# Performance work log

Measured on AMD Instinct MI355X. Metric: run time of the kernel, lower is better.

The kernel has to match this reference:

```python
import jax, jax.numpy as jnp
import numpy as np

N_NODES = 50000
N_EDGES = 800000
IN_C, HID_C, OUT_C = 256, 256, 128


def gcn_conv(x, W, b, row, col, n_nodes):
    """PyG GCNConv: linear transform, symmetric-normalized aggregation, bias.
    row/col already include self-loops. Messages flow row -> col."""
    h = x @ W  # [N, out]
    deg = jax.ops.segment_sum(jnp.ones_like(col, dtype=h.dtype), col, num_segments=n_nodes)
    d_inv_sqrt = jnp.where(deg > 0, jax.lax.rsqrt(jnp.maximum(deg, 1e-12)), 0.0)
    norm = d_inv_sqrt[row] * d_inv_sqrt[col]  # [E]
    msg = h[row] * norm[:, None]              # gather + scale, [E, out]
    out = jax.ops.segment_sum(msg, col, num_segments=n_nodes)  # scatter-add
    return out + b


def setup_inputs() -> dict:
    key = jax.random.key(0)
    k_x, k_e, k_w1, k_w2 = jax.random.split(key, 4)
    x = jax.random.normal(k_x, (N_NODES, IN_C), dtype=jnp.float32)
    edge_index = jax.random.randint(k_e, (2, N_EDGES), 0, N_NODES, dtype=jnp.int64)
    # Glorot-style init for GCN weights, zeros bias (PyG default)
    s1 = float(np.sqrt(6.0 / (IN_C + HID_C)))
    s2 = float(np.sqrt(6.0 / (HID_C + OUT_C)))
    W1 = jax.random.uniform(k_w1, (IN_C, HID_C), dtype=jnp.float32, minval=-s1, maxval=s1)
    b1 = jnp.zeros((HID_C,), dtype=jnp.float32)
    W2 = jax.random.uniform(k_w2, (HID_C, OUT_C), dtype=jnp.float32, minval=-s2, maxval=s2)
    b2 = jnp.zeros((OUT_C,), dtype=jnp.float32)
    return {"x": x, "edge_index": edge_index, "W1": W1, "b1": b1, "W2": W2, "b2": b2}


def reference(x, edge_index, W1, b1, W2, b2):
    n = x.shape[0]
    # add self-loops (PyG GCNConv default add_self_loops=True)
    loops = jnp.arange(n, dtype=edge_index.dtype)
    row = jnp.concatenate([edge_index[0], loops])
    col = jnp.concatenate([edge_index[1], loops])
    h = gcn_conv(x, W1, b1, row, col, n)
    h = jax.nn.relu(h)  # dropout p=0.0 -> identity
    out = gcn_conv(h, W2, b2, row, col, n)
    return out
```

## Files before the change

### kernel.cpp

```cpp
#include <hip/hip_runtime.h>

#define NN 50000
#define NE 800000
#define IN_C 256
#define HID_C 256
#define OUT_C 128

#define NBUCK 196
#define CHUNK 4096
#define NPA 196
#define CAP_B 5120

typedef unsigned short u16;
typedef __attribute__((ext_vector_type(8))) short short8;
typedef __attribute__((ext_vector_type(8))) unsigned short ushort8;
typedef __attribute__((ext_vector_type(4))) float f32x4;

__device__ __forceinline__ u16 f2b(float f) {
  unsigned int u = __float_as_uint(f);
  return (u16)((u + 0x7FFFu + ((u >> 16) & 1u)) >> 16);
}
__device__ __forceinline__ float b2f(u16 s) {
  return __uint_as_float(((unsigned int)s) << 16);
}


__global__ __launch_bounds__(256) void convw_zero(const float* __restrict__ W1,
                                                  const float* __restrict__ W2,
                                                  u16* __restrict__ W1t,
                                                  u16* __restrict__ W2t,
                                                  int* __restrict__ cnt,
                                                  u16* __restrict__ Hbz,
                                                  u16* __restrict__ H3z,
                                                  int nzb) {
  int b = blockIdx.x;
  if (b < 256) {
    int id = b * 256 + threadIdx.x;
    if (id < 256 * 256) {
      int n = id >> 8, k = id & 255;
      W1t[id] = f2b(W1[k * 256 + n]);
    }
    if (id < 128 * 256) {
      int n = id >> 8, k = id & 255;
      W2t[id] = f2b(W2[k * 128 + n]);
    }
  } else if (b < 256 + nzb) {
    int i = (b - 256) * 256 + threadIdx.x;
    if (i < NN) cnt[i] = 0;
  } else {
    if (threadIdx.x < 256) Hbz[threadIdx.x] = 0;
    if (threadIdx.x < 128) H3z[threadIdx.x] = 0;
  }
}


__global__ __launch_bounds__(256) void hist_kernel(const int* __restrict__ col,
                                                   int* __restrict__ cnt, int E) {
  int e = blockIdx.x * blockDim.x + threadIdx.x;
  if (e < E) atomicAdd(&cnt[col[e]], 1);
}

__global__ __launch_bounds__(256) void scan1_kernel(const int* __restrict__ cnt,
                                                    int* __restrict__ bsum, int n) {
  __shared__ int ws[4];
  int i = blockIdx.x * 256 + threadIdx.x;
  int lane = threadIdx.x & 63, wid = threadIdx.x >> 6;
  int v = (i < n) ? cnt[i] : 0;
#pragma unroll
  for (int off = 32; off > 0; off >>= 1) v += __shfl_down(v, off, 64);
  if (lane == 0) ws[wid] = v;
  __syncthreads();
  if (threadIdx.x == 0) bsum[blockIdx.x] = ws[0] + ws[1] + ws[2] + ws[3];
}

__global__ __launch_bounds__(256) void scan2_kernel(const int* __restrict__ bsum,
                                                    int* __restrict__ boff,
                                                    int* __restrict__ row_off,
                                                    int nb, int n) {
  __shared__ int wsum[4], wpre[5];
  int lane = threadIdx.x & 63, wid = threadIdx.x >> 6;
  int v = (threadIdx.x < nb) ? bsum[threadIdx.x] : 0;
  int s = v;
#pragma unroll
  for (int off = 1; off < 64; off <<= 1) {
    int t = __shfl_up(s, off, 64);
    if (lane >= off) s += t;
  }
  if (lane == 63) wsum[wid] = s;
  __syncthreads();
  if (threadIdx.x == 0) {
    int acc = 0;
#pragma unroll
    for (int w = 0; w < 4; ++w) { wpre[w] = acc; acc += wsum[w]; }
    wpre[4] = acc;
  }
  __syncthreads();
  if (threadIdx.x < nb) boff[threadIdx.x] = wpre[wid] + (s - v);
  if (threadIdx.x == 0) row_off[n] = wpre[4];
}

__global__ __launch_bounds__(256) void scan3_kernel(const int* __restrict__ cnt,
                                                    const int* __restrict__ boff,
                                                    int* __restrict__ row_off,
                                                    int* __restrict__ bcur,
                                                    float* __restrict__ dinv, int n) {
  __shared__ int wsum[4], wpre[4];
  int i = blockIdx.x * 256 + threadIdx.x;
  int lane = threadIdx.x & 63, wid = threadIdx.x >> 6;
  int v = (i < n) ? cnt[i] : 0;
  int s = v;
#pragma unroll
  for (int off = 1; off < 64; off <<= 1) {
    int t = __shfl_up(s, off, 64);
    if (lane >= off) s += t;
  }
  if (lane == 63) wsum[wid] = s;
  __syncthreads();
  if (threadIdx.x == 0) {
    int acc = 0;
#pragma unroll
    for (int w = 0; w < 4; ++w) { wpre[w] = acc; acc += wsum[w]; }
  }
  __syncthreads();
  if (i < n) {
    int off = boff[blockIdx.x] + wpre[wid] + (s - v);
    row_off[i] = off;
    if ((i & 255) == 0) bcur[i >> 8] = off;
    dinv[i] = rsqrtf((float)(v + 1));
  }
}


template <bool A_IS_F32>
__device__ __forceinline__ void gemm_body(const void* __restrict__ Ap,
                                          const u16* __restrict__ Bt,
                                          const float* __restrict__ dscale,
                                          u16* __restrict__ C, int M, int N,
                                          int bx, int by,
                                          u16 (&Asl)[2][5120], u16 (&Bsl)[2][5120]) {
  const int tid = threadIdx.x;
  const int row0 = by * 128;
  const int col0 = bx * 128;

  f32x4 acc[4][4] = {};

  const int seg = tid & 7;
  const int rb = tid >> 3;
  const int wave = tid >> 6, lane = tid & 63;
  const int wm = wave >> 1, wn = wave & 1;
  const int qr = lane & 15, quad = lane >> 4;

  float4 aF[4];
  ushort4 aU[4];
  ushort4 bR[4];

  auto load_tiles = [&](int k0) {
    if constexpr (A_IS_F32) {
      const float* A = (const float*)Ap;
#pragma unroll
      for (int i = 0; i < 4; ++i) {
        int gr = row0 + rb + i * 32;
        aF[i] = (gr < M) ? *(const float4*)&A[(size_t)gr * 256 + k0 + seg * 4]
                         : make_float4(0.f, 0.f, 0.f, 0.f);
      }
    } else {
      const u16* A = (const u16*)Ap;
#pragma unroll
      for (int i = 0; i < 4; ++i) {
        int gr = row0 + rb + i * 32;
        aU[i] = (gr < M) ? *(const ushort4*)&A[(size_t)gr * 256 + k0 + seg * 4]
                         : make_ushort4(0, 0, 0, 0);
      }
    }
#pragma unroll
    for (int i = 0; i < 4; ++i) {
      int n = rb + i * 32;
      bR[i] = *(const ushort4*)&Bt[(size_t)(col0 + n) * 256 + k0 + seg * 4];
    }
  };

  auto write_lds = [&](int buf) {
#pragma unroll
    for (int i = 0; i < 4; ++i) {
      int r = rb + i * 32;
      ushort4 u;
      if constexpr (A_IS_F32) {
        u.x = f2b(aF[i].x); u.y = f2b(aF[i].y);
        u.z = f2b(aF[i].z); u.w = f2b(aF[i].w);
      } else {
        u = aU[i];
      }
      *(ushort4*)&Asl[buf][r * 40 + seg * 4] = u;
      *(ushort4*)&Bsl[buf][r * 40 + seg * 4] = bR[i];
    }
  };

  load_tiles(0);
  write_lds(0);
  __syncthreads();

#pragma unroll
  for (int it = 0; it < 8; ++it) {
    const int cur = it & 1;
    if (it < 7) load_tiles((it + 1) * 32);

    short8 afr[4], bfr[4];
#pragma unroll
    for (int mt = 0; mt < 4; ++mt)
      afr[mt] = *(const short8*)&Asl[cur][(wm * 64 + mt * 16 + qr) * 40 + quad * 8];
#pragma unroll
    for (int nt = 0; nt < 4; ++nt)
      bfr[nt] = *(const short8*)&Bsl[cur][(wn * 64 + nt * 16 + qr) * 40 + quad * 8];
#pragma unroll
    for (int mt = 0; mt < 4; ++mt)
#pragma unroll
      for (int nt = 0; nt < 4; ++nt)
        acc[mt][nt] = __builtin_amdgcn_mfma_f32_16x16x32_bf16(afr[mt], bfr[nt], acc[mt][nt], 0, 0, 0);

    if (it < 7) {
      write_lds(1 - cur);
      __syncthreads();
    }
  }

#pragma unroll
  for (int mt = 0; mt < 4; ++mt) {
#pragma unroll
    for (int i = 0; i < 4; ++i) {
      int gr = row0 + wm * 64 + mt * 16 + quad * 4 + i;
      if (gr < M) {
        float sc = dscale[gr];
#pragma unroll
        for (int nt = 0; nt < 4; ++nt) {
          int gc = col0 + wn * 64 + nt * 16 + qr;
          C[(size_t)gr * N + gc] = f2b(acc[mt][nt][i] * sc);
        }
      }
    }
  }
}

template <bool A_IS_F32>
__global__ __launch_bounds__(256) void gemm_mfma(const void* __restrict__ Ap,
                                                 const u16* __restrict__ Bt,
                                                 const float* __restrict__ dscale,
                                                 u16* __restrict__ C, int M, int N) {
  __shared__ u16 Asl[2][5120];
  __shared__ u16 Bsl[2][5120];
  gemm_body<A_IS_F32>(Ap, Bt, dscale, C, M, N, blockIdx.x, blockIdx.y, Asl, Bsl);
}

__global__ __launch_bounds__(256) void gemm1_scatter(const float* __restrict__ x,
                                                     const u16* __restrict__ W1t,
                                                     const float* __restrict__ dinv,
                                                     u16* __restrict__ Hb, int M, int N,
                                                     int ngb,
                                                     const int* __restrict__ row,
                                                     const int* __restrict__ col,
                                                     int* __restrict__ bcur,
                                                     uint2* __restrict__ stage, int E) {
  __shared__ u16 ABsl[4][5120];
  int b = blockIdx.x;
  if (b < ngb) {
    gemm_body<true>(x, W1t, dinv, Hb, M, N, b & 1, b >> 1,
                    *reinterpret_cast<u16(*)[2][5120]>(&ABsl[0]),
                    *reinterpret_cast<u16(*)[2][5120]>(&ABsl[2]));
  } else {
    uint2* pairs = (uint2*)ABsl;
    int* hcnt = (int*)((char*)ABsl + 32768);
    int* hscan = hcnt + 256;
    int* hbase = hscan + 256;
    int* lcur = hbase + 256;

    const int tid = threadIdx.x;
    const int blk = b - ngb;
    const int e0 = blk * CHUNK;

    hcnt[tid] = 0;
    __syncthreads();

    int ecol[16], erow[16];
#pragma unroll
    for (int j = 0; j < 16; ++j) {
      int e = e0 + j * 256 + tid;
      if (e < E) {
        ecol[j] = col[e];
        erow[j] = row[e];
        atomicAdd(&hcnt[ecol[j] >> 8], 1);
      } else {
        ecol[j] = -1;
      }
    }
    __syncthreads();

    hscan[tid] = hcnt[tid];
    __syncthreads();
#pragma unroll
    for (int off = 1; off < 256; off <<= 1) {
      int t = (tid >= off) ? hscan[tid - off] : 0;
      __syncthreads();
      hscan[tid] += t;
      __syncthreads();
    }

    lcur[tid] = 0;
    if (hcnt[tid] > 0) hbase[tid] = atomicAdd(&bcur[tid], hcnt[tid]);
    __syncthreads();

#pragma unroll
    for (int j = 0; j < 16; ++j) {
      if (ecol[j] >= 0) {
        int bk = ecol[j] >> 8;
        int p = atomicAdd(&lcur[bk], 1);
        pairs[(hscan[bk] - hcnt[bk]) + p] = make_uint2((unsigned)erow[j], (unsigned)ecol[j]);
      }
    }
    __syncthreads();

    int mtot = hscan[255];
    for (int s = tid; s < mtot; s += 256) {
      uint2 pr = pairs[s];
      int bk = (int)(pr.y >> 8);
      stage[hbase[bk] + (s - (hscan[bk] - hcnt[bk]))] = pr;
    }
  }
}

__global__ __launch_bounds__(256) void csr_sort(const uint2* __restrict__ stage,
                                                const int* __restrict__ row_off,
                                                int* __restrict__ csr) {
  __shared__ int cur[256];
  __shared__ int outb[CAP_B];
  const int b = blockIdx.x;
  const int base_node = b << 8;
  const int nnodes = min(256, NN - base_node);
  const int tid = threadIdx.x;
  const int bstart = row_off[base_node];
  const int bend = row_off[min(base_node + 256, NN)];
  if (tid < nnodes) cur[tid] = row_off[base_node + tid] - bstart;
  __syncthreads();
  const int m = bend - bstart;
  for (int i = tid; i < m; i += 256) {
    uint2 pr = stage[bstart + i];
    int cl = (int)pr.y - base_node;
    int p = atomicAdd(&cur[cl], 1);
    if (p < CAP_B) outb[p] = (int)pr.x;
    else csr[bstart + p] = (int)pr.x;
  }
  __syncthreads();
  const int mm = min(m, CAP_B);
  for (int i = tid; i < mm; i += 256) csr[bstart + i] = outb[i];
}


__global__ __launch_bounds__(256) void agg256_bf(const u16* __restrict__ h,
                                                 const int* __restrict__ row_off,
                                                 const int* __restrict__ csr,
                                                 const float* __restrict__ dinv,
                                                 const float* __restrict__ bias,
                                                 u16* __restrict__ out, int n) {
  int wave = threadIdx.x >> 6;
  int lane = threadIdx.x & 63;
  int half = lane >> 5;
  int sl = lane & 31;
  int v = blockIdx.x * 4 + wave;
  if (v >= n) return;
  int beg = row_off[v], end = row_off[v + 1];
  ushort8 hs = *(const ushort8*)&h[(size_t)v * 256 + sl * 8];
  float a[8];
#pragma unroll
  for (int i = 0; i < 8; ++i) a[i] = half ? 0.f : b2f((u16)hs[i]);
  for (int e = beg; e < end; e += 16) {
    int p = e + (lane & 15);
    int idx = (p < end) ? csr[p] : NN;
    ushort8 g[8];
#pragma unroll
    for (int j = 0; j < 8; ++j) {
      int s = __shfl(idx, 2 * j + half, 64);
      g[j] = *(const ushort8*)&h[(size_t)s * 256 + sl * 8];
    }
#pragma unroll
    for (int j = 0; j < 8; ++j)
#pragma unroll
      for (int i = 0; i < 8; ++i) a[i] += b2f((u16)g[j][i]);
  }
#pragma unroll
  for (int i = 0; i < 8; ++i) a[i] += __shfl_xor(a[i], 32, 64);
  if (half == 0) {
    float dv = dinv[v];
    float4 bv0 = *(const float4*)&bias[sl * 8];
    float4 bv1 = *(const float4*)&bias[sl * 8 + 4];
    float bb[8] = {bv0.x, bv0.y, bv0.z, bv0.w, bv1.x, bv1.y, bv1.z, bv1.w};
    ushort8 o;
#pragma unroll
    for (int i = 0; i < 8; ++i) {
      float r = fmaxf(a[i] * dv + bb[i], 0.f);
      o[i] = (short)f2b(r);
    }
    *(ushort8*)&out[(size_t)v * 256 + sl * 8] = o;
  }
}

__global__ __launch_bounds__(256) void agg128_bf(const u16* __restrict__ h,
                                                 const int* __restrict__ row_off,
                                                 const int* __restrict__ csr,
                                                 const float* __restrict__ dinv,
                                                 const float* __restrict__ bias,
                                                 float* __restrict__ out, int n) {
  int wave = threadIdx.x >> 6;
  int lane = threadIdx.x & 63;
  int quarter = lane >> 4;
  int sl = lane & 15;
  int v = blockIdx.x * 4 + wave;
  if (v >= n) return;
  int beg = row_off[v], end = row_off[v + 1];
  ushort8 hs = *(const ushort8*)&h[(size_t)v * 128 + sl * 8];
  float a[8];
#pragma unroll
  for (int i = 0; i < 8; ++i) a[i] = quarter ? 0.f : b2f((u16)hs[i]);
  for (int e = beg; e < end; e += 16) {
    int p = e + (lane & 15);
    int idx = (p < end) ? csr[p] : NN;
    ushort8 g[4];
#pragma unroll
    for (int j = 0; j < 4; ++j) {
      int s = __shfl(idx, 4 * j + quarter, 64);
      g[j] = *(const ushort8*)&h[(size_t)s * 128 + sl * 8];
    }
#pragma unroll
    for (int j = 0; j < 4; ++j)
#pragma unroll
      for (int i = 0; i < 8; ++i) a[i] += b2f((u16)g[j][i]);
  }
#pragma unroll
  for (int i = 0; i < 8; ++i) {
    a[i] += __shfl_xor(a[i], 16, 64);
    a[i] += __shfl_xor(a[i], 32, 64);
  }
  if (quarter == 0 && (lane >> 5) == 0) {
    float dv = dinv[v];
    float4 bv0 = *(const float4*)&bias[sl * 8];
    float4 bv1 = *(const float4*)&bias[sl * 8 + 4];
    float bb[8] = {bv0.x, bv0.y, bv0.z, bv0.w, bv1.x, bv1.y, bv1.z, bv1.w};
    float o[8];
#pragma unroll
    for (int i = 0; i < 8; ++i) o[i] = a[i] * dv + bb[i];
    *(float4*)&out[(size_t)v * 128 + sl * 8] = make_float4(o[0], o[1], o[2], o[3]);
    *(float4*)&out[(size_t)v * 128 + sl * 8 + 4] = make_float4(o[4], o[5], o[6], o[7]);
  }
}


extern "C" void kernel_launch(void* const* d_in, const int* in_sizes, int n_in,
                              void* d_out, int out_size, void* d_ws, size_t ws_size,
                              hipStream_t stream) {
  const float* x = (const float*)d_in[0];
  const int* ei = (const int*)d_in[1];
  const float* W1 = (const float*)d_in[2];
  const float* b1 = (const float*)d_in[3];
  const float* W2 = (const float*)d_in[4];
  const float* b2 = (const float*)d_in[5];
  float* out = (float*)d_out;

  const int* row = ei;
  const int* col = ei + NE;

  const int NB = (NN + 255) / 256;

  u16* Hb = (u16*)d_ws;
  u16* H2b = Hb + (size_t)(NN + 1) * 256;
  u16* H3b = H2b + (size_t)NN * 256;
  u16* W1t = H3b + (size_t)(NN + 1) * 128;
  u16* W2t = W1t + 256 * 256;
  int* cnt = (int*)(W2t + 128 * 256);
  int* row_off = cnt + NN;
  int* bcur = row_off + NN + 4;
  float* dinv = (float*)(bcur + 256);
  int* bsum = (int*)(dinv + NN);
  int* boff = bsum + 200;
  int* csr = boff + 200;
  uint2* stage = (uint2*)H3b;

  convw_zero<<<256 + NB + 1, 256, 0, stream>>>(W1, W2, W1t, W2t, cnt,
                                               Hb + (size_t)NN * 256,
                                               H3b + (size_t)NN * 128, NB);
  hist_kernel<<<(NE + 255) / 256, 256, 0, stream>>>(col, cnt, NE);
  scan1_kernel<<<NB, 256, 0, stream>>>(cnt, bsum, NN);
  scan2_kernel<<<1, 256, 0, stream>>>(bsum, boff, row_off, NB, NN);
  scan3_kernel<<<NB, 256, 0, stream>>>(cnt, boff, row_off, bcur, dinv, NN);

  {
    const int ngb = (HID_C / 128) * ((NN + 127) / 128);
    gemm1_scatter<<<ngb + NPA, 256, 0, stream>>>(x, W1t, dinv, Hb, NN, HID_C, ngb,
                                                 row, col, bcur, stage, NE);
  }
  csr_sort<<<NBUCK, 256, 0, stream>>>(stage, row_off, csr);
  agg256_bf<<<(NN + 3) / 4, 256, 0, stream>>>(Hb, row_off, csr, dinv, b1, H2b, NN);

  {
    dim3 grid(OUT_C / 128, (NN + 127) / 128);
    gemm_mfma<false><<<grid, 256, 0, stream>>>(H2b, W2t, dinv, H3b, NN, OUT_C);
  }
  agg128_bf<<<(NN + 3) / 4, 256, 0, stream>>>(H3b, row_off, csr, dinv, b2, out, NN);
}
```

Measured before the change: 280.3 us.

## Split aggregation kernels into 64-channel slices across blocks with 8-edge lane groups

Replaces the two per-node aggregation kernels with one templated kernel that splits each node's feature row into 64-channel slices handled by separate blocks. Each wave processes 32 edges per iteration in 8 lane groups of 8 channel-lanes, then reduces across groups with shuffles. The aim is more parallelism and smaller per-wave gather footprints, but each node's row offsets and neighbour indices are now read once per slice. It also adds index clamping and bounds guards in csr_sort and the gathers.

```diff
diff --git a/kernel.cpp b/kernel.cpp
--- a/kernel.cpp
+++ b/kernel.cpp
@@ -342,10 +342,10 @@
   const int m = bend - bstart;
   for (int i = tid; i < m; i += 256) {
     uint2 pr = stage[bstart + i];
-    int cl = (int)pr.y - base_node;
+    int cl = min((int)pr.y - base_node, 255) & 255;
     int p = atomicAdd(&cur[cl], 1);
     if (p < CAP_B) outb[p] = (int)pr.x;
-    else csr[bstart + p] = (int)pr.x;
+    else if (bstart + p < NE) csr[bstart + p] = (int)pr.x;
   }
   __syncthreads();
   const int mm = min(m, CAP_B);
@@ -353,100 +353,72 @@
 }
 
 
-__global__ __launch_bounds__(256) void agg256_bf(const u16* __restrict__ h,
-                                                 const int* __restrict__ row_off,
-                                                 const int* __restrict__ csr,
-                                                 const float* __restrict__ dinv,
-                                                 const float* __restrict__ bias,
-                                                 u16* __restrict__ out, int n) {
-  int wave = threadIdx.x >> 6;
-  int lane = threadIdx.x & 63;
-  int half = lane >> 5;
-  int sl = lane & 31;
-  int v = blockIdx.x * 4 + wave;
+template <int ROW_CH, int NSL, bool RELU_BF16>
+__global__ __launch_bounds__(256) void agg_sliced(const u16* __restrict__ h,
+                                                  const int* __restrict__ row_off,
+                                                  const int* __restrict__ csr,
+                                                  const float* __restrict__ dinv,
+                                                  const float* __restrict__ bias,
+                                                  void* __restrict__ outp, int n) {
+  const int slice = blockIdx.x % NSL;
+  const int v = (blockIdx.x / NSL) * 4 + (threadIdx.x >> 6);
   if (v >= n) return;
-  int beg = row_off[v], end = row_off[v + 1];
-  ushort8 hs = *(const ushort8*)&h[(size_t)v * 256 + sl * 8];
-  float a[8];
-#pragma unroll
-  for (int i = 0; i < 8; ++i) a[i] = half ? 0.f : b2f((u16)hs[i]);
-  for (int e = beg; e < end; e += 16) {
-    int p = e + (lane & 15);
-    int idx = (p < end) ? csr[p] : NN;
-    ushort8 g[8];
-#pragma unroll
-    for (int j = 0; j < 8; ++j) {
-      int s = __shfl(idx, 2 * j + half, 64);
-      g[j] = *(const ushort8*)&h[(size_t)s * 256 + sl * 8];
-    }
-#pragma unroll
-    for (int j = 0; j < 8; ++j)
-#pragma unroll
-      for (int i = 0; i < 8; ++i) a[i] += b2f((u16)g[j][i]);
-  }
-#pragma unroll
-  for (int i = 0; i < 8; ++i) a[i] += __shfl_xor(a[i], 32, 64);
-  if (half == 0) {
-    float dv = dinv[v];
-    float4 bv0 = *(const float4*)&bias[sl * 8];
-    float4 bv1 = *(const float4*)&bias[sl * 8 + 4];
-    float bb[8] = {bv0.x, bv0.y, bv0.z, bv0.w, bv1.x, bv1.y, bv1.z, bv1.w};
-    ushort8 o;
+  const int lane = threadIdx.x & 63;
+  const int c = lane & 7;
+  const int eg = lane >> 3;
+  const int c0 = slice * 64 + c * 8;
+  const int beg = row_off[v], end = row_off[v + 1];
+
+  float a[8] = {};
+  for (int base = beg; base < end; base += 32) {
+    int p = base + (lane & 31);
+    int idx = (p < end) ? csr[min(p, NE - 1)] : NN;
+    idx = min((unsigned)idx, (unsigned)NN);
+    unsigned s0 = min((unsigned)__shfl(idx, 0 + eg, 64), (unsigned)NN);
+    unsigned s1 = min((unsigned)__shfl(idx, 8 + eg, 64), (unsigned)NN);
+    unsigned s2 = min((unsigned)__shfl(idx, 16 + eg, 64), (unsigned)NN);
+    unsigned s3 = min((unsigned)__shfl(idx, 24 + eg, 64), (unsigned)NN);
+    ushort8 g0 = *(const ushort8*)&h[(size_t)s0 * ROW_CH + c0];
+    ushort8 g1 = *(const ushort8*)&h[(size_t)s1 * ROW_CH + c0];
+    ushort8 g2 = *(const ushort8*)&h[(size_t)s2 * ROW_CH + c0];
+    ushort8 g3 = *(const ushort8*)&h[(size_t)s3 * ROW_CH + c0];
 #pragma unroll
     for (int i = 0; i < 8; ++i) {
-      float r = fmaxf(a[i] * dv + bb[i], 0.f);
-      o[i] = (short)f2b(r);
-    }
-    *(ushort8*)&out[(size_t)v * 256 + sl * 8] = o;
-  }
-}
-
-__global__ __launch_bounds__(256) void agg128_bf(const u16* __restrict__ h,
-                                                 const int* __restrict__ row_off,
-                                                 const int* __restrict__ csr,
-                                                 const float* __restrict__ dinv,
-                                                 const float* __restrict__ bias,
-                                                 float* __restrict__ out, int n) {
-  int wave = threadIdx.x >> 6;
-  int lane = threadIdx.x & 63;
-  int quarter = lane >> 4;
-  int sl = lane & 15;
-  int v = blockIdx.x * 4 + wave;
-  if (v >= n) return;
-  int beg = row_off[v], end = row_off[v + 1];
-  ushort8 hs = *(const ushort8*)&h[(size_t)v * 128 + sl * 8];
-  float a[8];
-#pragma unroll
-  for (int i = 0; i < 8; ++i) a[i] = quarter ? 0.f : b2f((u16)hs[i]);
-  for (int e = beg; e < end; e += 16) {
-    int p = e + (lane & 15);
-    int idx = (p < end) ? csr[p] : NN;
-    ushort8 g[4];
-#pragma unroll
-    for (int j = 0; j < 4; ++j) {
-      int s = __shfl(idx, 4 * j + quarter, 64);
-      g[j] = *(const ushort8*)&h[(size_t)s * 128 + sl * 8];
-    }
-#pragma unroll
-    for (int j = 0; j < 4; ++j)
-#pragma unroll
-      for (int i = 0; i < 8; ++i) a[i] += b2f((u16)g[j][i]);
+      a[i] += b2f((u16)g0[i]);
+      a[i] += b2f((u16)g1[i]);
+      a[i] += b2f((u16)g2[i]);
+      a[i] += b2f((u16)g3[i]);
+    }
   }
 #pragma unroll
   for (int i = 0; i < 8; ++i) {
+    a[i] += __shfl_xor(a[i], 8, 64);
     a[i] += __shfl_xor(a[i], 16, 64);
     a[i] += __shfl_xor(a[i], 32, 64);
   }
-  if (quarter == 0 && (lane >> 5) == 0) {
+  if (eg == 0) {
+    ushort8 hs = *(const ushort8*)&h[(size_t)v * ROW_CH + c0];
     float dv = dinv[v];
-    float4 bv0 = *(const float4*)&bias[sl * 8];
-    float4 bv1 = *(const float4*)&bias[sl * 8 + 4];
+    float4 bv0 = *(const float4*)&bias[c0];
+    float4 bv1 = *(const float4*)&bias[c0 + 4];
     float bb[8] = {bv0.x, bv0.y, bv0.z, bv0.w, bv1.x, bv1.y, bv1.z, bv1.w};
-    float o[8];
-#pragma unroll
-    for (int i = 0; i < 8; ++i) o[i] = a[i] * dv + bb[i];
-    *(float4*)&out[(size_t)v * 128 + sl * 8] = make_float4(o[0], o[1], o[2], o[3]);
-    *(float4*)&out[(size_t)v * 128 + sl * 8 + 4] = make_float4(o[4], o[5], o[6], o[7]);
+    if constexpr (RELU_BF16) {
+      u16* out = (u16*)outp;
+      ushort8 o;
+#pragma unroll
+      for (int i = 0; i < 8; ++i) {
+        float r = fmaxf((a[i] + b2f((u16)hs[i])) * dv + bb[i], 0.f);
+        o[i] = (short)f2b(r);
+      }
+      *(ushort8*)&out[(size_t)v * ROW_CH + c0] = o;
+    } else {
+      float* out = (float*)outp;
+      float o[8];
+#pragma unroll
+      for (int i = 0; i < 8; ++i) o[i] = (a[i] + b2f((u16)hs[i])) * dv + bb[i];
+      *(float4*)&out[(size_t)v * ROW_CH + c0] = make_float4(o[0], o[1], o[2], o[3]);
+      *(float4*)&out[(size_t)v * ROW_CH + c0 + 4] = make_float4(o[4], o[5], o[6], o[7]);
+    }
   }
 }
 
@@ -495,11 +467,15 @@
                                                  row, col, bcur, stage, NE);
   }
   csr_sort<<<NBUCK, 256, 0, stream>>>(stage, row_off, csr);
-  agg256_bf<<<(NN + 3) / 4, 256, 0, stream>>>(Hb, row_off, csr, dinv, b1, H2b, NN);
+
+  agg_sliced<256, 4, true><<<((NN + 3) / 4) * 4, 256, 0, stream>>>(
+      Hb, row_off, csr, dinv, b1, H2b, NN);
 
   {
     dim3 grid(OUT_C / 128, (NN + 127) / 128);
     gemm_mfma<false><<<grid, 256, 0, stream>>>(H2b, W2t, dinv, H3b, NN, OUT_C);
   }
-  agg128_bf<<<(NN + 3) / 4, 256, 0, stream>>>(H3b, row_off, csr, dinv, b2, out, NN);
-}
+
+  agg_sliced<128, 2, false><<<((NN + 3) / 4) * 2, 256, 0, stream>>>(
+      H3b, row_off, csr, dinv, b2, out, NN);
+}
```

New measurement: 305.4 us. +9.0%, slower.
